# Kernel tuning notes

Measured on AMD Instinct MI355X. Metric: run time of the kernel, lower is better.

The kernel has to match this reference:

```python
import jax, jax.numpy as jnp
import numpy as np
from jax import lax

IMG_H, IMG_W = 1024, 1536
N_IMG = 8
STRIDES = [4, 8, 16, 32, 64]
SIZES = [32, 64, 128, 256, 512]
RATIOS = np.array([0.5, 1.0, 2.0], dtype=np.float64)
A = 3
PRE_NMS_TOP_N = 1000
POST_NMS_TOP_N = 1000
NMS_THRESH = 0.7
SCORE_THRESH = 0.0
MIN_SIZE = 1e-3
BBOX_CLIP = float(np.log(1000.0 / 16.0))  # torchvision BoxCoder clamp on dw/dh
FEAT_SHAPES = [(IMG_H // s, IMG_W // s) for s in STRIDES]
NUM_PER_LEVEL = [h * w * A for h, w in FEAT_SHAPES]


def _make_anchors():
    # torchvision AnchorGenerator layout: per level, (h, w, anchor) order, matching permute_and_flatten
    out = []
    for (h, w), stride, size in zip(FEAT_SHAPES, STRIDES, SIZES):
        hr = np.sqrt(RATIOS)
        wr = 1.0 / hr
        base = np.stack([-wr * size, -hr * size, wr * size, hr * size], 1) / 2.0  # [A,4]
        sx = np.arange(w) * stride
        sy = np.arange(h) * stride
        gy, gx = np.meshgrid(sy, sx, indexing="ij")
        shifts = np.stack([gx, gy, gx, gy], -1).reshape(h, w, 1, 4)
        out.append((shifts + base.reshape(1, 1, A, 4)).reshape(-1, 4))
    return np.concatenate(out, 0).astype(np.float32)  # [T,4]


def setup_inputs() -> dict:
    key = jax.random.key(0)
    ks = jax.random.split(key, 10)
    inp = {}
    for i, (h, w) in enumerate(FEAT_SHAPES):
        inp[f"obj{i}"] = jax.random.normal(ks[i], (N_IMG, A, h, w), jnp.float32)
        inp[f"delta{i}"] = jax.random.normal(ks[5 + i], (N_IMG, A * 4, h, w), jnp.float32) * 0.5
    inp["anchors"] = jnp.asarray(_make_anchors())
    return inp


def _flatten_levels(objs, deltas):
    # permute_and_flatten: [N, A*C, H, W] -> [N, H*W*A, C]
    o_all, d_all = [], []
    for o, d in zip(objs, deltas):
        n, _, h, w = o.shape
        o_all.append(o.transpose(0, 2, 3, 1).reshape(n, -1))
        d_all.append(d.reshape(n, A, 4, h, w).transpose(0, 3, 4, 1, 2).reshape(n, -1, 4))
    return jnp.concatenate(o_all, 1), jnp.concatenate(d_all, 1)


def _decode(deltas, anchors):
    # BoxCoder(weights=(1,1,1,1)).decode
    wa = anchors[:, 2] - anchors[:, 0]
    ha = anchors[:, 3] - anchors[:, 1]
    cxa = anchors[:, 0] + 0.5 * wa
    cya = anchors[:, 1] + 0.5 * ha
    dx, dy = deltas[..., 0], deltas[..., 1]
    dw = jnp.minimum(deltas[..., 2], BBOX_CLIP)
    dh = jnp.minimum(deltas[..., 3], BBOX_CLIP)
    cx = dx * wa + cxa
    cy = dy * ha + cya
    pw = jnp.exp(dw) * wa
    ph = jnp.exp(dh) * ha
    return jnp.stack([cx - 0.5 * pw, cy - 0.5 * ph, cx + 0.5 * pw, cy + 0.5 * ph], -1)


def _box_iou(b1, b2):
    area1 = (b1[:, 2] - b1[:, 0]) * (b1[:, 3] - b1[:, 1])
    area2 = (b2[:, 2] - b2[:, 0]) * (b2[:, 3] - b2[:, 1])
    lt = jnp.maximum(b1[:, None, :2], b2[None, :, :2])
    rb = jnp.minimum(b1[:, None, 2:], b2[None, :, 2:])
    wh = jnp.clip(rb - lt, 0.0)
    inter = wh[..., 0] * wh[..., 1]
    return inter / (area1[:, None] + area2[None, :] - inter)


def _nms_one(boxes, nms_boxes, scores):
    # greedy NMS with fixed shapes; invalid entries carry score=-inf
    order = jnp.argsort(-scores)  # stable descending
    b, nb, s = boxes[order], nms_boxes[order], scores[order]
    iou = _box_iou(nb, nb)  # [K,K]
    k = s.shape[0]
    idxs = jnp.arange(k)
    valid = jnp.isfinite(s)

    def body(i, suppressed):
        keep_i = jnp.logical_not(suppressed[i]) & valid[i]
        return suppressed | (keep_i & (iou[i] > NMS_THRESH) & (idxs > i))

    suppressed = lax.fori_loop(0, k, body, jnp.zeros((k,), bool))
    keep = jnp.logical_not(suppressed) & valid
    sel = jnp.argsort(jnp.where(keep, 0, 1))[:POST_NMS_TOP_N]  # stable -> kept in score order
    kept = keep[sel]
    return jnp.where(kept[:, None], b[sel], 0.0), jnp.where(kept, s[sel], 0.0)


def reference(obj0, obj1, obj2, obj3, obj4, delta0, delta1, delta2, delta3, delta4, anchors):
    objs = [obj0, obj1, obj2, obj3, obj4]
    dels = [delta0, delta1, delta2, delta3, delta4]
    objectness, deltas = _flatten_levels(objs, dels)  # [N,T], [N,T,4]
    objectness = lax.stop_gradient(objectness)  # RPN detaches objectness and deltas
    deltas = lax.stop_gradient(deltas)
    proposals = _decode(deltas, anchors)  # [N,T,4]

    # per-level pre-NMS top-k, indices offset into the concatenated anchor axis
    lvl_full = jnp.concatenate([jnp.full((n,), i, jnp.int32) for i, n in enumerate(NUM_PER_LEVEL)])
    idx_parts, off = [], 0
    for n in NUM_PER_LEVEL:
        kk = min(PRE_NMS_TOP_N, n)
        _, ti = lax.top_k(objectness[:, off:off + n], kk)
        idx_parts.append(ti + off)
        off += n
    top_idx = jnp.concatenate(idx_parts, 1)  # [N,K]

    obj_sel = jnp.take_along_axis(objectness, top_idx, 1)
    boxes = jnp.take_along_axis(proposals, top_idx[..., None], 1)  # [N,K,4]
    lvl = lvl_full[top_idx]  # [N,K]
    scores = jax.nn.sigmoid(obj_sel)

    # clip to image
    x = jnp.clip(boxes[..., 0::2], 0.0, float(IMG_W))
    y = jnp.clip(boxes[..., 1::2], 0.0, float(IMG_H))
    boxes = jnp.stack([x[..., 0], y[..., 0], x[..., 1], y[..., 1]], -1)

    # remove_small_boxes + score threshold, as -inf score masking (fixed shapes)
    ok = ((boxes[..., 2] - boxes[..., 0]) >= MIN_SIZE) & ((boxes[..., 3] - boxes[..., 1]) >= MIN_SIZE)
    ok = ok & (scores >= SCORE_THRESH)
    scores_m = jnp.where(ok, scores, -jnp.inf)

    # batched_nms trick: shift boxes by level so different levels never overlap
    offset = lvl.astype(boxes.dtype) * (max(IMG_H, IMG_W) + 1.0)
    nms_boxes = boxes + offset[..., None]

    out_boxes, _ = jax.vmap(_nms_one)(boxes, nms_boxes, scores_m)
    return out_boxes  # [N_IMG, POST_NMS_TOP_N, 4], zero-padded
```

## Files before the change

### kernel.cpp

```cpp
#include <hip/hip_runtime.h>
#include <stdint.h>

#define N_IMGS 8
#define NLVL 5
#define TOT 392832
#define PRE_K 1000
#define POST_K 1000
#define KSEL 5000
#define MASKW 79
#define MROWS 5056
#define NCHUNK 79
#define LPAD 1024
#define MSLOTS (NLVL * LPAD)

typedef unsigned long long u64;

struct Ptrs {
    const float* obj[5];
    const float* del[5];
    const float* anch;
};

__device__ __forceinline__ unsigned flipf(float f) {
    unsigned u = __float_as_uint(f);
    return (u & 0x80000000u) ? ~u : (u | 0x80000000u);
}

__device__ __forceinline__ void lvl_info(int t, int& l, int& off, int& W, int& H) {
    if (t < 294912)      { l = 0; off = 0;      W = 384; H = 256; }
    else if (t < 368640) { l = 1; off = 294912; W = 192; H = 128; }
    else if (t < 387072) { l = 2; off = 368640; W = 96;  H = 64;  }
    else if (t < 391680) { l = 3; off = 387072; W = 48;  H = 32;  }
    else                 { l = 4; off = 391680; W = 24;  H = 16;  }
}

__device__ void decode_one(const Ptrs& P, int n, int t, float bx[4], bool& valid, int& lvl) {
#pragma clang fp contract(off)
    int l, off, W, H;
    lvl_info(t, l, off, W, H);
    lvl = l;
    int i = t - off;
    int a = i % 3;
    int p = i / 3;
    int y = p / W, x = p - y * W;
    const float* D = P.del[l];
    size_t plane = (size_t)W * H;
    size_t base = ((size_t)n * 12 + (size_t)a * 4) * plane + (size_t)y * W + x;
    float dx = D[base];
    float dy = D[base + plane];
    float dw = D[base + 2 * plane];
    float dh = D[base + 3 * plane];
    const float* an = P.anch + (size_t)t * 4;
    float a0 = an[0], a1 = an[1], a2 = an[2], a3 = an[3];
    float wa = a2 - a0, ha = a3 - a1;
    float cxa = a0 + 0.5f * wa, cya = a1 + 0.5f * ha;
    const float CLIP = 4.135166556742356f;
    dw = fminf(dw, CLIP);
    dh = fminf(dh, CLIP);
    float cx = dx * wa + cxa;
    float cy = dy * ha + cya;
    float pw = expf(dw) * wa;
    float ph = expf(dh) * ha;
    float x1 = cx - 0.5f * pw, y1 = cy - 0.5f * ph;
    float x2 = cx + 0.5f * pw, y2 = cy + 0.5f * ph;
    x1 = fminf(fmaxf(x1, 0.f), 1536.f);
    x2 = fminf(fmaxf(x2, 0.f), 1536.f);
    y1 = fminf(fmaxf(y1, 0.f), 1024.f);
    y2 = fminf(fmaxf(y2, 0.f), 1024.f);
    bx[0] = x1; bx[1] = y1; bx[2] = x2; bx[3] = y2;
    valid = ((x2 - x1) >= 1e-3f) && ((y2 - y1) >= 1e-3f);
}

__global__ void k_init(int* vcnt) {
    int i = threadIdx.x;
    if (i < N_IMGS) vcnt[i] = KSEL;
}

__global__ void k_zero_out(float* out, int n) {
    int i = blockIdx.x * blockDim.x + threadIdx.x;
    if (i < n) out[i] = 0.f;
}

__global__ void k_scores(Ptrs P, unsigned* scores) {
    int idx = blockIdx.x * blockDim.x + threadIdx.x;
    if (idx >= N_IMGS * TOT) return;
    int n = idx / TOT, t = idx - n * TOT;
    int l, off, W, H;
    lvl_info(t, l, off, W, H);
    int i = t - off;
    int a = i % 3;
    int p = i / 3;
    int y = p / W, x = p - y * W;
    const float* O = P.obj[l];
    float v = O[(((size_t)n * 3 + a) * H + y) * (size_t)W + x];
    scores[idx] = flipf(v);
}

#define HCOPY 4100
#define CANDMAX 4096
__global__ __launch_bounds__(1024) void k_select(const unsigned* scores, uint2* sel) {
    int task = blockIdx.x;
    int n = task / 5, l = task % 5;
    int off, len;
    switch (l) {
        case 0: off = 0;      len = 294912; break;
        case 1: off = 294912; len = 73728;  break;
        case 2: off = 368640; len = 18432;  break;
        case 3: off = 387072; len = 4608;   break;
        default: off = 391680; len = 1152;  break;
    }
    const unsigned* S = scores + (size_t)n * TOT + off;
    const uint4* S4 = (const uint4*)S;
    int len4 = len >> 2;
    int t = threadIdx.x;

    __shared__ __align__(16) char smem[2 * HCOPY * 4];
    unsigned* hist = (unsigned*)smem;
    unsigned long long* cand = (unsigned long long*)smem;
    __shared__ unsigned suf[1024];
    __shared__ unsigned sh_pivot, sh_krem;
    __shared__ int sh_ngt, sh_nc;

    for (int i = t; i < 2 * HCOPY; i += 1024) hist[i] = 0u;
    __syncthreads();

    unsigned* myh = hist + (t & 1) * HCOPY;
    for (int i = t; i < len4; i += 1024) {
        uint4 v = S4[i];
        atomicAdd(&myh[v.x >> 20], 1u);
        atomicAdd(&myh[v.y >> 20], 1u);
        atomicAdd(&myh[v.z >> 20], 1u);
        atomicAdd(&myh[v.w >> 20], 1u);
    }
    __syncthreads();
    for (int i = t; i < 4096; i += 1024) hist[i] += hist[HCOPY + i];
    __syncthreads();
    suf[t] = hist[4 * t] + hist[4 * t + 1] + hist[4 * t + 2] + hist[4 * t + 3];
    for (int d = 1; d < 1024; d <<= 1) {
        __syncthreads();
        unsigned v = (t + d < 1024) ? suf[t + d] : 0u;
        __syncthreads();
        suf[t] += v;
    }
    __syncthreads();
    unsigned above = (t == 1023) ? 0u : suf[t + 1];
    if (suf[t] >= PRE_K && above < PRE_K) {
        int b = 4 * t + 3;
        unsigned c = above;
        while (c + hist[b] < PRE_K) { c += hist[b]; --b; }
        sh_pivot = (unsigned)b;
        sh_krem = PRE_K - c;
        sh_ngt = 0; sh_nc = 0;
    }
    __syncthreads();
    unsigned pivot = sh_pivot;
    int krem = (int)sh_krem;
    __syncthreads();

    uint2* out = sel + (size_t)task * PRE_K;
    for (int i = t; i < len4; i += 1024) {
        uint4 v4 = S4[i];
        unsigned vv[4] = {v4.x, v4.y, v4.z, v4.w};
#pragma unroll
        for (int q = 0; q < 4; ++q) {
            unsigned v = vv[q];
            unsigned b = v >> 20;
            if (b > pivot) {
                int slot = atomicAdd(&sh_ngt, 1);
                out[slot] = make_uint2(v, (unsigned)(off + 4 * i + q));
            } else if (b == pivot) {
                int c = atomicAdd(&sh_nc, 1);
                if (c < CANDMAX)
                    cand[c] = ((unsigned long long)v << 32) | (unsigned)(off + 4 * i + q);
            }
        }
    }
    __syncthreads();
    int C = min(sh_nc, CANDMAX);
    int nbase = sh_ngt;
    for (int i = t; i < C; i += 1024) {
        unsigned long long a = cand[i];
        unsigned vi = (unsigned)(a >> 32), xi = (unsigned)a;
        int rank = 0;
        for (int j = 0; j < C; ++j) {
            unsigned long long bj = cand[j];
            unsigned vj = (unsigned)(bj >> 32), xj = (unsigned)bj;
            rank += (vj > vi) || (vj == vi && xj < xi);
        }
        if (rank < krem) out[nbase + rank] = make_uint2(vi, xi);
    }
}

__global__ void k_keys(Ptrs P, const uint2* sel, unsigned long long* keys) {
    int idx = blockIdx.x * blockDim.x + threadIdx.x;
    if (idx >= N_IMGS * KSEL) return;
    int n = idx / KSEL;
    uint2 s = sel[idx];
    float bx[4]; bool valid; int l;
    decode_one(P, n, (int)s.y, bx, valid, l);
    unsigned long long key;
    if (valid) key = ((unsigned long long)(~s.x) << 32) | (unsigned long long)s.y;
    else       key = 0xFFFFFFFF00000000ull | (unsigned long long)s.y;
    keys[idx] = key;
}

__global__ __launch_bounds__(1024) void k_sort1(const u64* keys, u64* keys2) {
    __shared__ u64 s[LPAD];
    int task = blockIdx.x;
    int n = task / 5, l = task % 5;
    int t = threadIdx.x;
    const u64* K = keys + (size_t)n * KSEL + (size_t)l * PRE_K;
    s[t] = (t < PRE_K) ? K[t] : ~0ull;
    for (int k = 2; k <= LPAD; k <<= 1) {
        for (int j = k >> 1; j > 0; j >>= 1) {
            __syncthreads();
            int ixj = t ^ j;
            if (ixj > t) {
                u64 a = s[t], b = s[ixj];
                bool asc = ((t & k) == 0);
                if (asc ? (a > b) : (a < b)) { s[t] = b; s[ixj] = a; }
            }
        }
    }
    __syncthreads();
    keys2[(size_t)task * LPAD + t] = s[t];
}

__global__ void k_merge(const u64* keys2, u64* keys) {
    int idx = blockIdx.x * blockDim.x + threadIdx.x;
    if (idx >= N_IMGS * MSLOTS) return;
    int n = idx / MSLOTS, slot = idx - n * MSLOTS;
    int l = slot >> 10, p = slot & (LPAD - 1);
    const u64* base = keys2 + (size_t)n * MSLOTS;
    u64 key = base[(size_t)l * LPAD + p];
    int rank = p;
#pragma unroll
    for (int m = 0; m < NLVL; ++m) {
        if (m == l) continue;
        const u64* L = base + (size_t)m * LPAD;
        bool le = (m < l);
        int lo = 0, hi = LPAD;
        while (lo < hi) {
            int mid = (lo + hi) >> 1;
            u64 v = L[mid];
            bool take = le ? (v <= key) : (v < key);
            if (take) lo = mid + 1; else hi = mid;
        }
        rank += lo;
    }
    if (rank < KSEL) keys[(size_t)n * KSEL + rank] = key;
}

__global__ void k_decode(Ptrs P, const unsigned long long* keys,
                         float4* boxes, float4* nboxes, int* vcnt) {
    int idx = blockIdx.x * blockDim.x + threadIdx.x;
    if (idx >= N_IMGS * KSEL) return;
    int n = idx / KSEL, r = idx - n * KSEL;
    unsigned long long key = keys[idx];
    if ((key >> 32) == 0xFFFFFFFFull) {
        boxes[idx] = make_float4(0.f, 0.f, 0.f, 0.f);
        nboxes[idx] = make_float4(0.f, 0.f, 0.f, 0.f);
        atomicMin(&vcnt[n], r);
        return;
    }
    int t = (int)(key & 0xFFFFFFFFull);
    float bx[4]; bool valid; int l;
    decode_one(P, n, t, bx, valid, l);
    boxes[idx] = make_float4(bx[0], bx[1], bx[2], bx[3]);
    float offv = (float)l * 1537.0f;
    nboxes[idx] = make_float4(bx[0] + offv, bx[1] + offv, bx[2] + offv, bx[3] + offv);
}

__global__ __launch_bounds__(64) void k_mask(const float4* nboxes, u64* maskT) {
#pragma clang fp contract(off)
    int rb = blockIdx.x, cb = blockIdx.y, n = blockIdx.z;
    if (cb < rb) return;
    __shared__ float4 cbox[64];
    int tid = threadIdx.x;
    int c0 = cb * 64;
    cbox[tid] = (c0 + tid < KSEL) ? nboxes[(size_t)n * KSEL + c0 + tid]
                                  : make_float4(0.f, 0.f, 0.f, 0.f);
    __syncthreads();
    int r = rb * 64 + tid;
    if (r >= KSEL) return;
    float4 rb4 = nboxes[(size_t)n * KSEL + r];
    float areaR = (rb4.z - rb4.x) * (rb4.w - rb4.y);
    u64 bits = 0ull;
    for (int cc = 0; cc < 64; ++cc) {
        int c = c0 + cc;
        if (c >= KSEL) break;
        if (c <= r) continue;
        float4 c4 = cbox[cc];
        float areaC = (c4.z - c4.x) * (c4.w - c4.y);
        float ltx = fmaxf(rb4.x, c4.x), lty = fmaxf(rb4.y, c4.y);
        float rbx = fminf(rb4.z, c4.z), rby = fminf(rb4.w, c4.w);
        float wv = fmaxf(rbx - ltx, 0.f), hv = fmaxf(rby - lty, 0.f);
        float inter = wv * hv;
        float iou = inter / (areaR + areaC - inter);
        if (iou > 0.7f) bits |= (1ull << cc);
    }
    maskT[((size_t)n * MASKW + cb) * MROWS + r] = bits;
}

__device__ __forceinline__ u64 bcast64(u64 v, int src) {
    unsigned lo = (unsigned)__builtin_amdgcn_readlane((int)(unsigned)v, src);
    unsigned hi = (unsigned)__builtin_amdgcn_readlane((int)(unsigned)(v >> 32), src);
    return ((u64)hi << 32) | (u64)lo;
}

__device__ __forceinline__ unsigned or_red_dpp(unsigned v) {
    v |= (unsigned)__builtin_amdgcn_update_dpp(0, (int)v, 0x111, 0xf, 0xf, true);
    v |= (unsigned)__builtin_amdgcn_update_dpp(0, (int)v, 0x112, 0xf, 0xf, true);
    v |= (unsigned)__builtin_amdgcn_update_dpp(0, (int)v, 0x114, 0xf, 0xf, true);
    v |= (unsigned)__builtin_amdgcn_update_dpp(0, (int)v, 0x118, 0xf, 0xf, true);
    v |= (unsigned)__builtin_amdgcn_update_dpp(0, (int)v, 0x142, 0xa, 0xf, false);
    v |= (unsigned)__builtin_amdgcn_update_dpp(0, (int)v, 0x143, 0xc, 0xf, false);
    return v;
}

__global__ __launch_bounds__(64, 1) void k_scan(const u64* maskT, const int* vcnt,
                                                int* keep, int* nkept) {
    __shared__ int keep_lds[1024];
    int n = blockIdx.x, lane = threadIdx.x;
    int V = vcnt[n];
    const u64* MT = maskT + (size_t)n * MASKW * MROWS;

    for (int i = lane; i < 1024; i += 64) keep_lds[i] = 0;

    int cnt = 0, cntprev = 0;
    u64 keptprev = 0ull;
    bool full = false;
    int nchunks = (V + 63) >> 6;

    u64 bulk[16];
#pragma unroll
    for (int q = 0; q < 16; ++q) bulk[q] = 0ull;
    u64 wc = MT[lane];
    u64 nc = 0ull;

    for (int c = 0; c < nchunks && !full; ++c) {
        u64 part = 0ull;
#pragma unroll
        for (int q = 0; q < 16; ++q)
            part |= (q * 64 + lane < cntprev) ? bulk[q] : 0ull;
        part |= ((keptprev >> lane) & 1ull) ? nc : 0ull;

        unsigned plo = or_red_dpp((unsigned)part);
        unsigned phi = or_red_dpp((unsigned)(part >> 32));
        u64 cur = ((u64)(unsigned)__builtin_amdgcn_readlane((int)phi, 63) << 32)
                | (u64)(unsigned)__builtin_amdgcn_readlane((int)plo, 63);

        int cntNow = cnt;
        int colN = (c + 1 < NCHUNK) ? (c + 1) : (NCHUNK - 1);
        const u64* colNp = MT + (size_t)colN * MROWS;
        {
            int kr[16];
#pragma unroll
            for (int q = 0; q < 16; ++q) kr[q] = keep_lds[q * 64 + lane];
#pragma unroll
            for (int q = 0; q < 16; ++q) bulk[q] = colNp[kr[q]];
        }
        u64 nc_next = colNp[(size_t)c * 64 + lane];
        u64 wc_next = colNp[(size_t)colN * 64 + lane];

        int base = c * 64;
        int jmax = V - base; if (jmax > 64) jmax = 64;
        u64 avail = ~cur;
        if (jmax < 64) avail &= (1ull << jmax) - 1ull;
        while (avail) {
            int j = __builtin_ctzll(avail);
            if (lane == 0) keep_lds[cnt] = base + j;
            ++cnt;
            if (cnt == POST_K) { full = true; break; }
            u64 wcj = bcast64(wc, j);
            avail &= avail - 1;
            avail &= ~wcj;
        }
        keptprev = 0ull;
        for (int i = cntNow + (int)lane; i < cnt; i += 64) {
            int r = keep_lds[i];
            keptprev |= 1ull << (r - base);
        }
        {
            unsigned klo = or_red_dpp((unsigned)keptprev);
            unsigned khi = or_red_dpp((unsigned)(keptprev >> 32));
            keptprev = ((u64)(unsigned)__builtin_amdgcn_readlane((int)khi, 63) << 32)
                     | (u64)(unsigned)__builtin_amdgcn_readlane((int)klo, 63);
        }
        cntprev = cntNow;
        wc = wc_next;
        nc = nc_next;
    }

    for (int i = lane; i < cnt; i += 64) keep[n * POST_K + i] = keep_lds[i];
    if (lane == 0) nkept[n] = cnt;
}

__global__ void k_out(const float4* boxes, const int* keep, const int* nkept, float4* out) {
    int idx = blockIdx.x * blockDim.x + threadIdx.x;
    if (idx >= N_IMGS * POST_K) return;
    int n = idx / POST_K, k = idx - n * POST_K;
    float4 v = make_float4(0.f, 0.f, 0.f, 0.f);
    if (k < nkept[n]) v = boxes[(size_t)n * KSEL + keep[n * POST_K + k]];
    out[idx] = v;
}

extern "C" void kernel_launch(void* const* d_in, const int* in_sizes, int n_in,
                              void* d_out, int out_size, void* d_ws, size_t ws_size,
                              hipStream_t stream) {
    Ptrs P;
    for (int l = 0; l < 5; ++l) {
        P.obj[l] = (const float*)d_in[2 * l];
        P.del[l] = (const float*)d_in[2 * l + 1];
    }
    P.anch = (const float*)d_in[10];

    size_t o = 0;
    auto alloc = [&](size_t bytes) {
        size_t cur = o;
        o = (o + bytes + 255) & ~(size_t)255;
        return cur;
    };
    size_t off_scores = alloc((size_t)N_IMGS * TOT * 4);
    size_t off_sel    = alloc((size_t)N_IMGS * KSEL * 8);
    size_t off_keys   = alloc((size_t)N_IMGS * KSEL * 8);
    size_t off_keys2  = alloc((size_t)N_IMGS * MSLOTS * 8);
    size_t off_boxes  = alloc((size_t)N_IMGS * KSEL * 16);
    size_t off_nbox   = alloc((size_t)N_IMGS * KSEL * 16);
    size_t off_mask   = alloc((size_t)N_IMGS * MASKW * MROWS * 8);
    size_t off_vcnt   = alloc(N_IMGS * 4);
    size_t off_keep   = alloc((size_t)N_IMGS * POST_K * 4);
    size_t off_nkept  = alloc(N_IMGS * 4);

    float* out = (float*)d_out;
    if (o > ws_size) {
        k_zero_out<<<(out_size + 255) / 256, 256, 0, stream>>>(out, out_size);
        return;
    }

    char* w = (char*)d_ws;
    unsigned* scores          = (unsigned*)(w + off_scores);
    uint2* sel                = (uint2*)(w + off_sel);
    unsigned long long* keys  = (unsigned long long*)(w + off_keys);
    u64* keys2                = (u64*)(w + off_keys2);
    float4* boxes             = (float4*)(w + off_boxes);
    float4* nboxes            = (float4*)(w + off_nbox);
    u64* maskT                = (u64*)(w + off_mask);
    int* vcnt                 = (int*)(w + off_vcnt);
    int* keep                 = (int*)(w + off_keep);
    int* nkept                = (int*)(w + off_nkept);

    k_init<<<1, 32, 0, stream>>>(vcnt);
    k_scores<<<(N_IMGS * TOT + 255) / 256, 256, 0, stream>>>(P, scores);
    k_select<<<N_IMGS * NLVL, 1024, 0, stream>>>(scores, sel);
    k_keys<<<(N_IMGS * KSEL + 255) / 256, 256, 0, stream>>>(P, sel, keys);
    k_sort1<<<N_IMGS * NLVL, 1024, 0, stream>>>(keys, keys2);
    k_merge<<<(N_IMGS * MSLOTS + 255) / 256, 256, 0, stream>>>(keys2, keys);
    k_decode<<<(N_IMGS * KSEL + 255) / 256, 256, 0, stream>>>(P, keys, boxes, nboxes, vcnt);
    k_mask<<<dim3(NCHUNK, MASKW, N_IMGS), 64, 0, stream>>>(nboxes, maskT);
    k_scan<<<N_IMGS, 64, 0, stream>>>(maskT, vcnt, keep, nkept);
    k_out<<<(N_IMGS * POST_K + 255) / 256, 256, 0, stream>>>((const float4*)boxes, keep, nkept, (float4*)d_out);
}
```

Before: 360.8 us.

## Fuse init/keys/merge/decode kernels and rewrite IoU mask with wave ballots

Folds the vcnt init into k_scores, the key computation into the per-level sort, and the merge with the box decode, removing three launches and the intermediate keys buffer. The IoU mask kernel now broadcasts row boxes via readlane and builds each 64-bit mask word with a ballot, dropping the LDS stage and the per-thread serial bit loop. It also replaces the division with a multiplicative threshold test, falling back to a true divide only near the boundary. The risks are rounding mismatches around the threshold and more readlane traffic.

```diff
diff --git a/kernel.cpp b/kernel.cpp
--- a/kernel.cpp
+++ b/kernel.cpp
@@ -71,17 +71,13 @@
     valid = ((x2 - x1) >= 1e-3f) && ((y2 - y1) >= 1e-3f);
 }
 
-__global__ void k_init(int* vcnt) {
-    int i = threadIdx.x;
-    if (i < N_IMGS) vcnt[i] = KSEL;
-}
-
 __global__ void k_zero_out(float* out, int n) {
     int i = blockIdx.x * blockDim.x + threadIdx.x;
     if (i < n) out[i] = 0.f;
 }
 
-__global__ void k_scores(Ptrs P, unsigned* scores) {
+__global__ void k_scores(Ptrs P, unsigned* scores, int* vcnt) {
+    if (blockIdx.x == 0 && threadIdx.x < N_IMGS) vcnt[threadIdx.x] = KSEL;
     int idx = blockIdx.x * blockDim.x + threadIdx.x;
     if (idx >= N_IMGS * TOT) return;
     int n = idx / TOT, t = idx - n * TOT;
@@ -191,26 +187,20 @@
     }
 }
 
-__global__ void k_keys(Ptrs P, const uint2* sel, unsigned long long* keys) {
-    int idx = blockIdx.x * blockDim.x + threadIdx.x;
-    if (idx >= N_IMGS * KSEL) return;
-    int n = idx / KSEL;
-    uint2 s = sel[idx];
-    float bx[4]; bool valid; int l;
-    decode_one(P, n, (int)s.y, bx, valid, l);
-    unsigned long long key;
-    if (valid) key = ((unsigned long long)(~s.x) << 32) | (unsigned long long)s.y;
-    else       key = 0xFFFFFFFF00000000ull | (unsigned long long)s.y;
-    keys[idx] = key;
-}
-
-__global__ __launch_bounds__(1024) void k_sort1(const u64* keys, u64* keys2) {
+__global__ __launch_bounds__(1024) void k_sort1(Ptrs P, const uint2* sel, u64* keys2) {
     __shared__ u64 s[LPAD];
     int task = blockIdx.x;
-    int n = task / 5, l = task % 5;
+    int n = task / 5;
     int t = threadIdx.x;
-    const u64* K = keys + (size_t)n * KSEL + (size_t)l * PRE_K;
-    s[t] = (t < PRE_K) ? K[t] : ~0ull;
+    u64 key = ~0ull;
+    if (t < PRE_K) {
+        uint2 sv = sel[(size_t)task * PRE_K + t];
+        float bx[4]; bool valid; int lv;
+        decode_one(P, n, (int)sv.y, bx, valid, lv);
+        key = valid ? (((u64)(~sv.x) << 32) | (u64)sv.y)
+                    : (0xFFFFFFFF00000000ull | (u64)sv.y);
+    }
+    s[t] = key;
     for (int k = 2; k <= LPAD; k <<= 1) {
         for (int j = k >> 1; j > 0; j >>= 1) {
             __syncthreads();
@@ -226,13 +216,15 @@
     keys2[(size_t)task * LPAD + t] = s[t];
 }
 
-__global__ void k_merge(const u64* keys2, u64* keys) {
+__global__ void k_mergedec(Ptrs P, const u64* keys2,
+                           float4* boxes, float4* nboxes, int* vcnt) {
     int idx = blockIdx.x * blockDim.x + threadIdx.x;
     if (idx >= N_IMGS * MSLOTS) return;
     int n = idx / MSLOTS, slot = idx - n * MSLOTS;
     int l = slot >> 10, p = slot & (LPAD - 1);
     const u64* base = keys2 + (size_t)n * MSLOTS;
     u64 key = base[(size_t)l * LPAD + p];
+    if (key == ~0ull) return;
     int rank = p;
 #pragma unroll
     for (int m = 0; m < NLVL; ++m) {
@@ -248,58 +240,63 @@
         }
         rank += lo;
     }
-    if (rank < KSEL) keys[(size_t)n * KSEL + rank] = key;
-}
-
-__global__ void k_decode(Ptrs P, const unsigned long long* keys,
-                         float4* boxes, float4* nboxes, int* vcnt) {
-    int idx = blockIdx.x * blockDim.x + threadIdx.x;
-    if (idx >= N_IMGS * KSEL) return;
-    int n = idx / KSEL, r = idx - n * KSEL;
-    unsigned long long key = keys[idx];
+    if (rank >= KSEL) return;
+    int oidx = n * KSEL + rank;
     if ((key >> 32) == 0xFFFFFFFFull) {
-        boxes[idx] = make_float4(0.f, 0.f, 0.f, 0.f);
-        nboxes[idx] = make_float4(0.f, 0.f, 0.f, 0.f);
-        atomicMin(&vcnt[n], r);
+        boxes[oidx] = make_float4(0.f, 0.f, 0.f, 0.f);
+        nboxes[oidx] = make_float4(0.f, 0.f, 0.f, 0.f);
+        atomicMin(&vcnt[n], rank);
         return;
     }
     int t = (int)(key & 0xFFFFFFFFull);
-    float bx[4]; bool valid; int l;
-    decode_one(P, n, t, bx, valid, l);
-    boxes[idx] = make_float4(bx[0], bx[1], bx[2], bx[3]);
-    float offv = (float)l * 1537.0f;
-    nboxes[idx] = make_float4(bx[0] + offv, bx[1] + offv, bx[2] + offv, bx[3] + offv);
-}
-
-__global__ __launch_bounds__(64) void k_mask(const float4* nboxes, u64* maskT) {
+    float bx[4]; bool valid; int lv;
+    decode_one(P, n, t, bx, valid, lv);
+    boxes[oidx] = make_float4(bx[0], bx[1], bx[2], bx[3]);
+    float offv = (float)lv * 1537.0f;
+    nboxes[oidx] = make_float4(bx[0] + offv, bx[1] + offv, bx[2] + offv, bx[3] + offv);
+}
+
+__global__ __launch_bounds__(64) void k_mask(const float4* __restrict__ nboxes,
+                                             u64* __restrict__ maskT) {
 #pragma clang fp contract(off)
     int rb = blockIdx.x, cb = blockIdx.y, n = blockIdx.z;
     if (cb < rb) return;
-    __shared__ float4 cbox[64];
-    int tid = threadIdx.x;
-    int c0 = cb * 64;
-    cbox[tid] = (c0 + tid < KSEL) ? nboxes[(size_t)n * KSEL + c0 + tid]
-                                  : make_float4(0.f, 0.f, 0.f, 0.f);
-    __syncthreads();
-    int r = rb * 64 + tid;
-    if (r >= KSEL) return;
-    float4 rb4 = nboxes[(size_t)n * KSEL + r];
-    float areaR = (rb4.z - rb4.x) * (rb4.w - rb4.y);
-    u64 bits = 0ull;
-    for (int cc = 0; cc < 64; ++cc) {
-        int c = c0 + cc;
-        if (c >= KSEL) break;
-        if (c <= r) continue;
-        float4 c4 = cbox[cc];
-        float areaC = (c4.z - c4.x) * (c4.w - c4.y);
-        float ltx = fmaxf(rb4.x, c4.x), lty = fmaxf(rb4.y, c4.y);
-        float rbx = fminf(rb4.z, c4.z), rby = fminf(rb4.w, c4.w);
-        float wv = fmaxf(rbx - ltx, 0.f), hv = fmaxf(rby - lty, 0.f);
+    int lane = threadIdx.x;
+    int r0 = rb * 64, c0 = cb * 64;
+    const float4 z4 = make_float4(0.f, 0.f, 0.f, 0.f);
+    float4 cbx = (c0 + lane < KSEL) ? nboxes[(size_t)n * KSEL + c0 + lane] : z4;
+    float4 rbx = (r0 + lane < KSEL) ? nboxes[(size_t)n * KSEL + r0 + lane] : z4;
+    float areaC = (cbx.z - cbx.x) * (cbx.w - cbx.y);
+    float areaR = (rbx.z - rbx.x) * (rbx.w - rbx.y);
+    u64 colmask = __ballot(c0 + lane < KSEL);
+    bool diag = (rb == cb);
+    u64 myword = 0ull;
+    for (int rr = 0; rr < 64; ++rr) {
+        float rx1 = __int_as_float(__builtin_amdgcn_readlane(__float_as_int(rbx.x), rr));
+        float ry1 = __int_as_float(__builtin_amdgcn_readlane(__float_as_int(rbx.y), rr));
+        float rx2 = __int_as_float(__builtin_amdgcn_readlane(__float_as_int(rbx.z), rr));
+        float ry2 = __int_as_float(__builtin_amdgcn_readlane(__float_as_int(rbx.w), rr));
+        float aR  = __int_as_float(__builtin_amdgcn_readlane(__float_as_int(areaR), rr));
+        float ltx = fmaxf(rx1, cbx.x), lty = fmaxf(ry1, cbx.y);
+        float rbxx = fminf(rx2, cbx.z), rbyy = fminf(ry2, cbx.w);
+        float wv = fmaxf(rbxx - ltx, 0.f), hv = fmaxf(rbyy - lty, 0.f);
         float inter = wv * hv;
-        float iou = inter / (areaR + areaC - inter);
-        if (iou > 0.7f) bits |= (1ull << cc);
-    }
-    maskT[((size_t)n * MASKW + cb) * MROWS + r] = bits;
+        float uni = (aR + areaC) - inter;
+        float ta = 0.7f * uni;
+        bool hi = inter > ta * 1.000002f;
+        bool lo = inter < ta * 0.999998f;
+        bool sup = hi;
+        bool mid = !(hi || lo);
+        if (__any((int)mid)) {
+            float d = inter / uni;
+            sup = mid ? (d > 0.7f) : sup;
+        }
+        if (diag) sup = sup && (lane > rr);
+        u64 w = __ballot((int)sup) & colmask;
+        myword = (lane == rr) ? w : myword;
+    }
+    if (r0 + lane < KSEL)
+        maskT[((size_t)n * MASKW + cb) * MROWS + r0 + lane] = myword;
 }
 
 __device__ __forceinline__ u64 bcast64(u64 v, int src) {
@@ -423,7 +420,6 @@
     };
     size_t off_scores = alloc((size_t)N_IMGS * TOT * 4);
     size_t off_sel    = alloc((size_t)N_IMGS * KSEL * 8);
-    size_t off_keys   = alloc((size_t)N_IMGS * KSEL * 8);
     size_t off_keys2  = alloc((size_t)N_IMGS * MSLOTS * 8);
     size_t off_boxes  = alloc((size_t)N_IMGS * KSEL * 16);
     size_t off_nbox   = alloc((size_t)N_IMGS * KSEL * 16);
@@ -439,24 +435,20 @@
     }
 
     char* w = (char*)d_ws;
-    unsigned* scores          = (unsigned*)(w + off_scores);
-    uint2* sel                = (uint2*)(w + off_sel);
-    unsigned long long* keys  = (unsigned long long*)(w + off_keys);
-    u64* keys2                = (u64*)(w + off_keys2);
-    float4* boxes             = (float4*)(w + off_boxes);
-    float4* nboxes            = (float4*)(w + off_nbox);
-    u64* maskT                = (u64*)(w + off_mask);
-    int* vcnt                 = (int*)(w + off_vcnt);
-    int* keep                 = (int*)(w + off_keep);
-    int* nkept                = (int*)(w + off_nkept);
-
-    k_init<<<1, 32, 0, stream>>>(vcnt);
-    k_scores<<<(N_IMGS * TOT + 255) / 256, 256, 0, stream>>>(P, scores);
+    unsigned* scores = (unsigned*)(w + off_scores);
+    uint2* sel       = (uint2*)(w + off_sel);
+    u64* keys2       = (u64*)(w + off_keys2);
+    float4* boxes    = (float4*)(w + off_boxes);
+    float4* nboxes   = (float4*)(w + off_nbox);
+    u64* maskT       = (u64*)(w + off_mask);
+    int* vcnt        = (int*)(w + off_vcnt);
+    int* keep        = (int*)(w + off_keep);
+    int* nkept       = (int*)(w + off_nkept);
+
+    k_scores<<<(N_IMGS * TOT + 255) / 256, 256, 0, stream>>>(P, scores, vcnt);
     k_select<<<N_IMGS * NLVL, 1024, 0, stream>>>(scores, sel);
-    k_keys<<<(N_IMGS * KSEL + 255) / 256, 256, 0, stream>>>(P, sel, keys);
-    k_sort1<<<N_IMGS * NLVL, 1024, 0, stream>>>(keys, keys2);
-    k_merge<<<(N_IMGS * MSLOTS + 255) / 256, 256, 0, stream>>>(keys2, keys);
-    k_decode<<<(N_IMGS * KSEL + 255) / 256, 256, 0, stream>>>(P, keys, boxes, nboxes, vcnt);
+    k_sort1<<<N_IMGS * NLVL, 1024, 0, stream>>>(P, sel, keys2);
+    k_mergedec<<<(N_IMGS * MSLOTS + 255) / 256, 256, 0, stream>>>(P, keys2, boxes, nboxes, vcnt);
     k_mask<<<dim3(NCHUNK, MASKW, N_IMGS), 64, 0, stream>>>(nboxes, maskT);
     k_scan<<<N_IMGS, 64, 0, stream>>>(maskT, vcnt, keep, nkept);
     k_out<<<(N_IMGS * POST_K + 255) / 256, 256, 0, stream>>>((const float4*)boxes, keep, nkept, (float4*)d_out);
```

New measurement: 370.3 us. 2.6% more time.
